# Kernel optimization log

Measured on AMD Instinct MI355X. Metric: run time of the kernel, lower is better.

The kernel has to match this reference:

```python
import jax, jax.numpy as jnp
import numpy as np
import math

V = 50257   # target_vocab_size
E = 512     # opt.out_embeddings_size
B = 8
L = 2048
NR = 100    # noise_ratio
NORM_TERM = math.log(V)   # norm_term='auto'
LOG_NR = math.log(NR)


def setup_inputs() -> dict:
    key = jax.random.key(0)
    k1, k2, k3, k4, k5 = jax.random.split(key, 5)
    # build_unigram_noise: counts -> probs; clamp(1e-10); renorm; log  (Zipf-like counts)
    counts = 1.0 / np.arange(1, V + 1, dtype=np.float64)
    probs = counts / counts.sum()
    probs = np.clip(probs, 1e-10, None)
    probs = probs / probs.sum()
    logprob_noise = jnp.asarray(np.log(probs), dtype=jnp.float32)
    target = jax.random.randint(k1, (B, L), 0, V)
    noise_idx = jax.random.randint(k2, (NR,), 0, V)  # shared noise (per_word=False)
    inp = jax.random.normal(k3, (B, L, E), jnp.float32) * 0.05
    emb_weight = jax.random.normal(k4, (V, E), jnp.float32) * 0.02
    bias_weight = jax.random.normal(k5, (V,), jnp.float32) * 0.01
    return {"input": inp, "emb_weight": emb_weight, "bias_weight": bias_weight,
            "logprob_noise": logprob_noise, "target": target, "noise_idx": noise_idx}


def reference(input, emb_weight, bias_weight, logprob_noise, target, noise_idx):
    # _compute_sampled_logit_batched
    flat_in = input.reshape(-1, E)                    # (B*L, E)
    tflat = target.reshape(-1)                        # (B*L,)
    t_emb = emb_weight[tflat]                         # gather (B*L, E)
    target_score = jnp.sum(flat_in * t_emb, axis=1) + bias_weight[tflat]
    n_emb = emb_weight[noise_idx]                     # (NR, E)
    noise_score = flat_in @ n_emb.T + bias_weight[noise_idx]  # (B*L, NR)
    # _get_logit: subtract norm term
    logit_t_model = target_score.reshape(B, L) - NORM_TERM
    logit_n_model = noise_score.reshape(B, L, NR) - NORM_TERM
    # noise-distribution log-probs
    logit_t_noise = logprob_noise[target]                                   # (B, L)
    logit_n_noise = jnp.broadcast_to(logprob_noise[noise_idx], (B, L, NR))  # shared
    # nce_loss
    logit_model = jnp.concatenate([logit_t_model[..., None], logit_n_model], axis=2)
    logit_noise = jnp.concatenate([logit_t_noise[..., None], logit_n_noise], axis=2)
    x = logit_model - logit_noise - LOG_NR            # (B, L, NR+1)
    # BCEWithLogits, label=1 at slot 0 else 0: loss = softplus(x) - x*y
    bce = jnp.logaddexp(0.0, x)
    bce = bce.at[:, :, 0].add(-x[:, :, 0])
    loss = bce.sum(axis=2)                            # (B, L)
    return loss.mean()                                # reduction='elementwise_mean'
```

## Files before the change

kernel.cpp:

```cpp
#include <hip/hip_runtime.h>

#define E_SZ   512
#define NROWS  16384
#define NR     100
#define NW     112
#define MT     32
#define KC     64
#define STR    72
#define NCHUNK (E_SZ / KC)

typedef __attribute__((ext_vector_type(8))) short short8;
typedef __attribute__((ext_vector_type(4))) float f32x4;

__device__ __forceinline__ unsigned short f2bf(float f) {
    unsigned int u = __float_as_uint(f);
    u += 0x7FFFu + ((u >> 16) & 1u);
    return (unsigned short)(u >> 16);
}
__device__ __forceinline__ float bf2f(unsigned short h) {
    return __uint_as_float(((unsigned int)h) << 16);
}
__device__ __forceinline__ float softplus(float x) {
    return fmaxf(x, 0.f) + log1pf(__expf(-fabsf(x)));
}
__device__ __forceinline__ short8 cvt8(float4 a, float4 b) {
    short8 v;
    v[0] = (short)f2bf(a.x); v[1] = (short)f2bf(a.y);
    v[2] = (short)f2bf(a.z); v[3] = (short)f2bf(a.w);
    v[4] = (short)f2bf(b.x); v[5] = (short)f2bf(b.y);
    v[6] = (short)f2bf(b.z); v[7] = (short)f2bf(b.w);
    return v;
}

__global__ __launch_bounds__(256, 2)
void nce_loss_kernel(const float* __restrict__ inp,
                     const float* __restrict__ emb,
                     const float* __restrict__ bias,
                     const float* __restrict__ lpn,
                     const int*   __restrict__ target,
                     const int*   __restrict__ nidx,
                     float* __restrict__ out)
{
    const float NTL = (float)(10.824907387009307 + 4.605170185988091);

    const int t  = threadIdx.x;
    const int r0 = blockIdx.x * MT;

    __shared__ __align__(16) unsigned short sIn[MT * STR];
    __shared__ __align__(16) unsigned short sNs[NW * STR];
    __shared__ float sBn[NW];
    __shared__ float sTb[MT];
    __shared__ int   sTg[MT];
    __shared__ int   sNi[NW];
    __shared__ float sRed[MT * 8];
    __shared__ float sWs[4];

    if (t < NW) {
        int idx = (t < NR) ? nidx[t] : 0;
        sNi[t] = idx;
        sBn[t] = (t < NR) ? (bias[idx] - NTL - lpn[idx]) : 0.f;
    }
    if (t < MT) {
        int tg = target[r0 + t];
        sTg[t] = tg;
        sTb[t] = bias[tg] - NTL - lpn[tg];
    }
    __syncthreads();

    const int rr = t >> 3;
    const int kg = t & 7;
    float tacc = 0.f;

    const int w     = t >> 6;
    const int lane  = t & 63;
    const int c     = lane & 15;
    const int q     = lane >> 4;
    const int mrow  = (w >> 1) * 16 + c;
    const int half  = w & 1;
    const int ntcnt = half ? 3 : 4;
    const int nbase = half * 4;

    f32x4 acc[4];
#pragma unroll
    for (int i = 0; i < 4; ++i) acc[i] = {0.f, 0.f, 0.f, 0.f};

    const float* inRow = inp + (size_t)(r0 + rr) * E_SZ + kg * 8;
    const float* tgRow = emb + (size_t)sTg[rr] * E_SZ + kg * 8;

    for (int kc = 0; kc < NCHUNK; ++kc) {
        const int k0 = kc * KC;

        {
            float4 x0 = *(const float4*)(inRow + k0);
            float4 x1 = *(const float4*)(inRow + k0 + 4);
            *(short8*)&sIn[rr * STR + kg * 8] = cvt8(x0, x1);
        }
        for (int task = t; task < NW * 8; task += 256) {
            int j = task >> 3, g = task & 7;
            short8 v = {0, 0, 0, 0, 0, 0, 0, 0};
            if (j < NR) {
                const float* p = emb + (size_t)sNi[j] * E_SZ + k0 + g * 8;
                float4 x0 = *(const float4*)p;
                float4 x1 = *(const float4*)(p + 4);
                v = cvt8(x0, x1);
            }
            *(short8*)&sNs[j * STR + g * 8] = v;
        }
        __syncthreads();

        {
            float4 e0 = *(const float4*)(tgRow + k0);
            float4 e1 = *(const float4*)(tgRow + k0 + 4);
            short8 iv = *(const short8*)&sIn[rr * STR + kg * 8];
            tacc += bf2f((unsigned short)iv[0]) * e0.x
                  + bf2f((unsigned short)iv[1]) * e0.y
                  + bf2f((unsigned short)iv[2]) * e0.z
                  + bf2f((unsigned short)iv[3]) * e0.w
                  + bf2f((unsigned short)iv[4]) * e1.x
                  + bf2f((unsigned short)iv[5]) * e1.y
                  + bf2f((unsigned short)iv[6]) * e1.z
                  + bf2f((unsigned short)iv[7]) * e1.w;
        }

#pragma unroll
        for (int k32 = 0; k32 < 2; ++k32) {
            const int ko = k32 * 32 + q * 8;
            short8 A = *(const short8*)&sIn[mrow * STR + ko];
#pragma unroll
            for (int ti = 0; ti < 4; ++ti) {
                if (ti < ntcnt) {
                    short8 Bv = *(const short8*)&sNs[((nbase + ti) * 16 + c) * STR + ko];
                    acc[ti] = __builtin_amdgcn_mfma_f32_16x16x32_bf16(A, Bv, acc[ti], 0, 0, 0);
                }
            }
        }
        __syncthreads();
    }

    float ll = 0.f;
#pragma unroll
    for (int ti = 0; ti < 4; ++ti) {
        if (ti < ntcnt) {
            int word = (nbase + ti) * 16 + c;
            if (word < NR) {
                float bn = sBn[word];
#pragma unroll
                for (int i = 0; i < 4; ++i) {
                    ll += softplus(acc[ti][i] + bn);
                }
            }
        }
    }

    sRed[t] = tacc;
    __syncthreads();
    if (t < MT) {
        float s = 0.f;
#pragma unroll
        for (int i = 0; i < 8; ++i) s += sRed[t * 8 + i];
        float xt = s + sTb[t];
        ll += softplus(-xt);
    }

#pragma unroll
    for (int off = 32; off > 0; off >>= 1) ll += __shfl_down(ll, off);
    if (lane == 0) sWs[w] = ll;
    __syncthreads();
    if (t == 0) {
        float s = (sWs[0] + sWs[1]) + (sWs[2] + sWs[3]);
        atomicAdd(out, s * (1.f / (float)NROWS));
    }
}

extern "C" void kernel_launch(void* const* d_in, const int* in_sizes, int n_in,
                              void* d_out, int out_size, void* d_ws, size_t ws_size,
                              hipStream_t stream) {
    const float* inp    = (const float*)d_in[0];
    const float* emb    = (const float*)d_in[1];
    const float* bias   = (const float*)d_in[2];
    const float* lpn    = (const float*)d_in[3];
    const int*   target = (const int*)d_in[4];
    const int*   nidx   = (const int*)d_in[5];
    float* out = (float*)d_out;

    hipMemsetAsync(out, 0, sizeof(float), stream);
    nce_loss_kernel<<<NROWS / MT, 256, 0, stream>>>(inp, emb, bias, lpn, target, nidx, out);
}
```

Before: 194.7 us.

## Split K across waves with direct-register MFMA operands and LDS atomic reduction

Replaces the chunked LDS-staged GEMM with a split-K scheme. Each wave loads its 128-wide K slice of the input, target and noise embeddings straight from global memory into MFMA registers, with no per-chunk barriers. The target dot product now also runs on MFMA, using the diagonal of a 16x16 tile. Partial accumulators are reduced through LDS float atomics before the softplus epilogue. The float-to-bf16 conversion moves to a perm-based packing that rounds differently (round-half-up instead of round-to-nearest-even). In exchange there are redundant global loads of the noise rows per wave, 14 of 16 MFMAs wasted on the target diagonal, and extra atomic traffic in LDS.

```diff
diff --git a/kernel.cpp b/kernel.cpp
--- a/kernel.cpp
+++ b/kernel.cpp
@@ -1,35 +1,30 @@
 #include <hip/hip_runtime.h>
+
 
 #define E_SZ   512
 #define NROWS  16384
-#define NR     100
-#define NW     112
+#define NRn    100
 #define MT     32
-#define KC     64
-#define STR    72
-#define NCHUNK (E_SZ / KC)
+#define KW     128
 
 typedef __attribute__((ext_vector_type(8))) short short8;
 typedef __attribute__((ext_vector_type(4))) float f32x4;
 
-__device__ __forceinline__ unsigned short f2bf(float f) {
-    unsigned int u = __float_as_uint(f);
-    u += 0x7FFFu + ((u >> 16) & 1u);
-    return (unsigned short)(u >> 16);
+__device__ __forceinline__ unsigned int pack2(float a, float b) {
+    unsigned int ua = __float_as_uint(a) + 0x8000u;
+    unsigned int ub = __float_as_uint(b) + 0x8000u;
+    return __builtin_amdgcn_perm(ub, ua, 0x07060302u);
 }
-__device__ __forceinline__ float bf2f(unsigned short h) {
-    return __uint_as_float(((unsigned int)h) << 16);
+__device__ __forceinline__ short8 cvt8(float4 x0, float4 x1) {
+    union { unsigned int u[4]; short8 s; } r;
+    r.u[0] = pack2(x0.x, x0.y);
+    r.u[1] = pack2(x0.z, x0.w);
+    r.u[2] = pack2(x1.x, x1.y);
+    r.u[3] = pack2(x1.z, x1.w);
+    return r.s;
 }
 __device__ __forceinline__ float softplus(float x) {
     return fmaxf(x, 0.f) + log1pf(__expf(-fabsf(x)));
-}
-__device__ __forceinline__ short8 cvt8(float4 a, float4 b) {
-    short8 v;
-    v[0] = (short)f2bf(a.x); v[1] = (short)f2bf(a.y);
-    v[2] = (short)f2bf(a.z); v[3] = (short)f2bf(a.w);
-    v[4] = (short)f2bf(b.x); v[5] = (short)f2bf(b.y);
-    v[6] = (short)f2bf(b.z); v[7] = (short)f2bf(b.w);
-    return v;
 }
 
 __global__ __launch_bounds__(256, 2)
@@ -41,125 +36,108 @@
                      const int*   __restrict__ nidx,
                      float* __restrict__ out)
 {
-    const float NTL = (float)(10.824907387009307 + 4.605170185988091);
+    const float NTL = 15.430077572997398f;
 
-    const int t  = threadIdx.x;
-    const int r0 = blockIdx.x * MT;
+    const int t    = threadIdx.x;
+    const int w    = t >> 6;
+    const int lane = t & 63;
+    const int c    = lane & 15;
+    const int q    = lane >> 4;
+    const int r0   = blockIdx.x * MT;
 
-    __shared__ __align__(16) unsigned short sIn[MT * STR];
-    __shared__ __align__(16) unsigned short sNs[NW * STR];
-    __shared__ float sBn[NW];
-    __shared__ float sTb[MT];
-    __shared__ int   sTg[MT];
-    __shared__ int   sNi[NW];
-    __shared__ float sRed[MT * 8];
+    __shared__ float sAcc[16 * 4 * 64];
+    __shared__ float sBn[112];
+    __shared__ float sTb[32];
     __shared__ float sWs[4];
 
-    if (t < NW) {
-        int idx = (t < NR) ? nidx[t] : 0;
-        sNi[t] = idx;
-        sBn[t] = (t < NR) ? (bias[idx] - NTL - lpn[idx]) : 0.f;
+    for (int i = t; i < 4096; i += 256) sAcc[i] = 0.f;
+    if (t < 112) {
+        int idx = (t < NRn) ? nidx[t] : 0;
+        sBn[t] = (t < NRn) ? (bias[idx] - NTL - lpn[idx]) : 0.f;
     }
-    if (t < MT) {
+    if (t < 32) {
         int tg = target[r0 + t];
-        sTg[t] = tg;
         sTb[t] = bias[tg] - NTL - lpn[tg];
+    }
+
+    const float* pA0 = inp + (size_t)(r0 + c) * E_SZ;
+    const float* pA1 = inp + (size_t)(r0 + 16 + c) * E_SZ;
+    const float* pT0 = emb + (size_t)target[r0 + c] * E_SZ;
+    const float* pT1 = emb + (size_t)target[r0 + 16 + c] * E_SZ;
+    const float* pN[7];
+#pragma unroll
+    for (int ti = 0; ti < 7; ++ti) {
+        int wd = ti * 16 + c;
+        int ix = (wd < NRn) ? nidx[wd] : 0;
+        pN[ti] = emb + (size_t)ix * E_SZ;
+    }
+
+    f32x4 accN[2][7];
+    f32x4 accT[2];
+#pragma unroll
+    for (int mt = 0; mt < 2; ++mt) {
+        accT[mt] = {0.f, 0.f, 0.f, 0.f};
+#pragma unroll
+        for (int ti = 0; ti < 7; ++ti) accN[mt][ti] = {0.f, 0.f, 0.f, 0.f};
+    }
+
+    const int kbase = w * KW + q * 8;
+
+#pragma unroll
+    for (int ks = 0; ks < KW / 32; ++ks) {
+        const int k = kbase + ks * 32;
+        short8 A0 = cvt8(*(const float4*)(pA0 + k), *(const float4*)(pA0 + k + 4));
+        short8 A1 = cvt8(*(const float4*)(pA1 + k), *(const float4*)(pA1 + k + 4));
+        short8 T0 = cvt8(*(const float4*)(pT0 + k), *(const float4*)(pT0 + k + 4));
+        short8 T1 = cvt8(*(const float4*)(pT1 + k), *(const float4*)(pT1 + k + 4));
+        accT[0] = __builtin_amdgcn_mfma_f32_16x16x32_bf16(A0, T0, accT[0], 0, 0, 0);
+        accT[1] = __builtin_amdgcn_mfma_f32_16x16x32_bf16(A1, T1, accT[1], 0, 0, 0);
+#pragma unroll
+        for (int ti = 0; ti < 7; ++ti) {
+            short8 Bv = cvt8(*(const float4*)(pN[ti] + k), *(const float4*)(pN[ti] + k + 4));
+            accN[0][ti] = __builtin_amdgcn_mfma_f32_16x16x32_bf16(A0, Bv, accN[0][ti], 0, 0, 0);
+            accN[1][ti] = __builtin_amdgcn_mfma_f32_16x16x32_bf16(A1, Bv, accN[1][ti], 0, 0, 0);
+        }
+    }
+
+    __syncthreads();
+#pragma unroll
+    for (int mt = 0; mt < 2; ++mt) {
+#pragma unroll
+        for (int ti = 0; ti < 7; ++ti) {
+#pragma unroll
+            for (int r = 0; r < 4; ++r)
+                atomicAdd(&sAcc[((mt * 7 + ti) * 4 + r) * 64 + lane], accN[mt][ti][r]);
+        }
+#pragma unroll
+        for (int r = 0; r < 4; ++r)
+            atomicAdd(&sAcc[((14 + mt) * 4 + r) * 64 + lane], accT[mt][r]);
     }
     __syncthreads();
 
-    const int rr = t >> 3;
-    const int kg = t & 7;
-    float tacc = 0.f;
-
-    const int w     = t >> 6;
-    const int lane  = t & 63;
-    const int c     = lane & 15;
-    const int q     = lane >> 4;
-    const int mrow  = (w >> 1) * 16 + c;
-    const int half  = w & 1;
-    const int ntcnt = half ? 3 : 4;
-    const int nbase = half * 4;
-
-    f32x4 acc[4];
+    const int tr   = t >> 2;
+    const int tile = tr >> 2;
+    const int reg  = tr & 3;
+    const int lb   = (t & 3) * 16;
+    float ll = 0.f;
+    if (tile < 14) {
+        const int ti = (tile < 7) ? tile : tile - 7;
 #pragma unroll
-    for (int i = 0; i < 4; ++i) acc[i] = {0.f, 0.f, 0.f, 0.f};
-
-    const float* inRow = inp + (size_t)(r0 + rr) * E_SZ + kg * 8;
-    const float* tgRow = emb + (size_t)sTg[rr] * E_SZ + kg * 8;
-
-    for (int kc = 0; kc < NCHUNK; ++kc) {
-        const int k0 = kc * KC;
-
-        {
-            float4 x0 = *(const float4*)(inRow + k0);
-            float4 x1 = *(const float4*)(inRow + k0 + 4);
-            *(short8*)&sIn[rr * STR + kg * 8] = cvt8(x0, x1);
+        for (int i = 0; i < 16; ++i) {
+            int ln = lb + i;
+            int word = ti * 16 + (ln & 15);
+            if (word < NRn)
+                ll += softplus(sAcc[tr * 64 + ln] + sBn[word]);
         }
-        for (int task = t; task < NW * 8; task += 256) {
-            int j = task >> 3, g = task & 7;
-            short8 v = {0, 0, 0, 0, 0, 0, 0, 0};
-            if (j < NR) {
-                const float* p = emb + (size_t)sNi[j] * E_SZ + k0 + g * 8;
-                float4 x0 = *(const float4*)p;
-                float4 x1 = *(const float4*)(p + 4);
-                v = cvt8(x0, x1);
-            }
-            *(short8*)&sNs[j * STR + g * 8] = v;
+    } else {
+        const int mt = tile - 14;
+        const int row = (lb >> 4) * 4 + reg;
+#pragma unroll
+        for (int i = 0; i < 16; ++i) {
+            int ln = lb + i;
+            if ((ln & 15) == row)
+                ll += softplus(-(sAcc[tr * 64 + ln] + sTb[mt * 16 + row]));
         }
-        __syncthreads();
-
-        {
-            float4 e0 = *(const float4*)(tgRow + k0);
-            float4 e1 = *(const float4*)(tgRow + k0 + 4);
-            short8 iv = *(const short8*)&sIn[rr * STR + kg * 8];
-            tacc += bf2f((unsigned short)iv[0]) * e0.x
-                  + bf2f((unsigned short)iv[1]) * e0.y
-                  + bf2f((unsigned short)iv[2]) * e0.z
-                  + bf2f((unsigned short)iv[3]) * e0.w
-                  + bf2f((unsigned short)iv[4]) * e1.x
-                  + bf2f((unsigned short)iv[5]) * e1.y
-                  + bf2f((unsigned short)iv[6]) * e1.z
-                  + bf2f((unsigned short)iv[7]) * e1.w;
-        }
-
-#pragma unroll
-        for (int k32 = 0; k32 < 2; ++k32) {
-            const int ko = k32 * 32 + q * 8;
-            short8 A = *(const short8*)&sIn[mrow * STR + ko];
-#pragma unroll
-            for (int ti = 0; ti < 4; ++ti) {
-                if (ti < ntcnt) {
-                    short8 Bv = *(const short8*)&sNs[((nbase + ti) * 16 + c) * STR + ko];
-                    acc[ti] = __builtin_amdgcn_mfma_f32_16x16x32_bf16(A, Bv, acc[ti], 0, 0, 0);
-                }
-            }
-        }
-        __syncthreads();
-    }
-
-    float ll = 0.f;
-#pragma unroll
-    for (int ti = 0; ti < 4; ++ti) {
-        if (ti < ntcnt) {
-            int word = (nbase + ti) * 16 + c;
-            if (word < NR) {
-                float bn = sBn[word];
-#pragma unroll
-                for (int i = 0; i < 4; ++i) {
-                    ll += softplus(acc[ti][i] + bn);
-                }
-            }
-        }
-    }
-
-    sRed[t] = tacc;
-    __syncthreads();
-    if (t < MT) {
-        float s = 0.f;
-#pragma unroll
-        for (int i = 0; i < 8; ++i) s += sRed[t * 8 + i];
-        float xt = s + sTb[t];
-        ll += softplus(-xt);
     }
 
 #pragma unroll
```

After: 225.9 us. 16.0% more time.
